# Performance work log

Hardware: AMD Instinct MI355X
Metric: run time of the kernel (lower is better)

The kernel has to match this reference:

```python
import jax, jax.numpy as jnp
import numpy as np

NUM_IN, IN_DIM, NUM_OUT, OUT_DIM, NUM_ROUTING = 1152, 8, 10, 16, 3
BATCH = 256


def squash(v):
    # v: (..., d). scale = |v|^2/(1+|v|^2) * v/|v|
    sq = jnp.sum(v * v, axis=-1, keepdims=True)
    scale = sq / (1.0 + sq)
    return scale * v / jnp.sqrt(sq + 1e-8)


def setup_inputs() -> dict:
    key = jax.random.key(0)
    k1, k2 = jax.random.split(key)
    input_capsules = jax.random.normal(k1, (BATCH, NUM_IN, IN_DIM), dtype=jnp.float32)
    W = jax.random.normal(k2, (NUM_IN, IN_DIM, NUM_OUT, OUT_DIM), dtype=jnp.float32) * 0.01
    return {"input_capsules": input_capsules, "W": W}


def reference(input_capsules, W):
    # u_hat: (b, i, j, o) -- predictions from each input capsule i for output capsule j
    u_hat = jnp.einsum('bid,idjo->bijo', input_capsules, W)
    b = jnp.zeros(u_hat.shape[:3] + (1,), dtype=u_hat.dtype)  # (b, i, j, 1)
    v = None
    for it in range(NUM_ROUTING):
        c = jax.nn.softmax(b, axis=2)                 # coupling coeffs over output capsules j
        s = jnp.sum(c * u_hat, axis=1)                # (b, j, o)
        v = squash(s)                                 # (b, j, o)
        if it < NUM_ROUTING - 1:
            agreement = jnp.sum(u_hat * v[:, None, :, :], axis=-1, keepdims=True)
            b = b + agreement
    return v
```

## Files before the change

### kernel.cpp

```cpp
#include <hip/hip_runtime.h>


#define NUM_IN 1152
#define NUM_OUT 10
#define OUT_DIM 16
#define BATCH 256
#define SLOTS 160
#define ICH_BLK 16
#define NCHUNK (NUM_IN / ICH_BLK)
#define BPB 16
#define NBT (BATCH / BPB)
#define WROW 1280

typedef unsigned int __attribute__((address_space(1))) as1_uint;
typedef unsigned int __attribute__((address_space(3))) as3_uint;
typedef int v2i __attribute__((ext_vector_type(2)));

__device__ __forceinline__ void gll16(const float* g, float* l) {
  __builtin_amdgcn_global_load_lds((const as1_uint*)g, (as3_uint*)l, 16, 0, 0);
}

__device__ __forceinline__ float xor8_sum(float x) {
  int v = __builtin_amdgcn_update_dpp(0, __float_as_int(x), 0x128, 0xF, 0xF, true);
  return x + __int_as_float(v);
}

__device__ __forceinline__ float xor32_sum(float x) {
  v2i r = __builtin_amdgcn_permlane32_swap(__float_as_int(x),
                                           __float_as_int(x), false, false);
  return __int_as_float(r.x) + __int_as_float(r.y);
}

__device__ __forceinline__ float rowsum8_hi(float x) {
  int v;
  v = __builtin_amdgcn_update_dpp(0, __float_as_int(x), 0x114, 0xF, 0xF, true);
  x += __int_as_float(v);
  v = __builtin_amdgcn_update_dpp(0, __float_as_int(x), 0x112, 0xF, 0xF, true);
  x += __int_as_float(v);
  v = __builtin_amdgcn_update_dpp(0, __float_as_int(x), 0x111, 0xF, 0xF, true);
  x += __int_as_float(v);
  return x;
}

__device__ __forceinline__ float rowsum16(float x) {
  int v;
  v = __builtin_amdgcn_update_dpp(0, __float_as_int(x), 0x128, 0xF, 0xF, true);
  x += __int_as_float(v);
  v = __builtin_amdgcn_update_dpp(0, __float_as_int(x), 0x124, 0xF, 0xF, true);
  x += __int_as_float(v);
  v = __builtin_amdgcn_update_dpp(0, __float_as_int(x), 0x122, 0xF, 0xF, true);
  x += __int_as_float(v);
  v = __builtin_amdgcn_update_dpp(0, __float_as_int(x), 0x121, 0xF, 0xF, true);
  x += __int_as_float(v);
  return x;
}

template <int PASS, int R, bool PART>
__device__ __forceinline__ void compute_round(
    const float4 xv[2][2], const float* __restrict__ v0p,
    const float* __restrict__ v1p, float* __restrict__ outp, const float* Wb,
    int b0, int lane, int vbase, size_t obase) {
  constexpr size_t BBS = PART ? (size_t)(NCHUNK * SLOTS) : (size_t)SLOTS;
  const float* wsl = Wb + lane * 4;

  float xd[2][8];
#pragma unroll
  for (int bb = 0; bb < 2; ++bb) {
    xd[bb][0] = xv[bb][0].x; xd[bb][1] = xv[bb][0].y;
    xd[bb][2] = xv[bb][0].z; xd[bb][3] = xv[bb][0].w;
    xd[bb][4] = xv[bb][1].x; xd[bb][5] = xv[bb][1].y;
    xd[bb][6] = xv[bb][1].z; xd[bb][7] = xv[bb][1].w;
  }

  float u[2][5][4];
  float cw[2][5];

#pragma unroll
  for (int jl = 0; jl < 5; ++jl) {
    float ax0 = 0.f, ay0 = 0.f, az0 = 0.f, aw0 = 0.f;
    float ax1 = 0.f, ay1 = 0.f, az1 = 0.f, aw1 = 0.f;
#pragma unroll
    for (int d = 0; d < 8; ++d) {
      const float4 w =
          *reinterpret_cast<const float4*>(wsl + (d * 5 + jl) * 256);
      ax0 = fmaf(xd[0][d], w.x, ax0); ay0 = fmaf(xd[0][d], w.y, ay0);
      az0 = fmaf(xd[0][d], w.z, az0); aw0 = fmaf(xd[0][d], w.w, aw0);
      ax1 = fmaf(xd[1][d], w.x, ax1); ay1 = fmaf(xd[1][d], w.y, ay1);
      az1 = fmaf(xd[1][d], w.z, az1); aw1 = fmaf(xd[1][d], w.w, aw1);
    }
    u[0][jl][0] = ax0; u[0][jl][1] = ay0; u[0][jl][2] = az0; u[0][jl][3] = aw0;
    u[1][jl][0] = ax1; u[1][jl][1] = ay1; u[1][jl][2] = az1; u[1][jl][3] = aw1;
    if (PASS >= 1) {
#pragma unroll
      for (int bb = 0; bb < 2; ++bb) {
        const float4 p = *reinterpret_cast<const float4*>(
            v0p + (b0 + bb) * SLOTS + vbase + jl * 16);
        float lgv = u[bb][jl][0] * p.x + u[bb][jl][1] * p.y +
                    u[bb][jl][2] * p.z + u[bb][jl][3] * p.w;
        if (PASS == 2) {
          const float4 q = *reinterpret_cast<const float4*>(
              v1p + (b0 + bb) * SLOTS + vbase + jl * 16);
          lgv += u[bb][jl][0] * q.x + u[bb][jl][1] * q.y +
                 u[bb][jl][2] * q.z + u[bb][jl][3] * q.w;
        }
        cw[bb][jl] = xor32_sum(xor8_sum(lgv));
      }
    }
  }

  if (PASS == 0) {
#pragma unroll
    for (int bb = 0; bb < 2; ++bb)
#pragma unroll
      for (int jl = 0; jl < 5; ++jl) cw[bb][jl] = 0.1f;
  } else {
#pragma unroll
    for (int bb = 0; bb < 2; ++bb) {
      float m = cw[bb][0];
#pragma unroll
      for (int jl = 1; jl < 5; ++jl) m = fmaxf(m, cw[bb][jl]);
      m = fmaxf(m, __shfl_xor(m, 16));
      float z = 0.f;
#pragma unroll
      for (int jl = 0; jl < 5; ++jl) {
        cw[bb][jl] = __expf(cw[bb][jl] - m);
        z += cw[bb][jl];
      }
      z += __shfl_xor(z, 16);
      const float rz = 1.0f / z;
#pragma unroll
      for (int jl = 0; jl < 5; ++jl) cw[bb][jl] *= rz;
    }
  }

  const bool wr = ((lane & 7) == 7);
#pragma unroll
  for (int jl = 0; jl < 5; ++jl) {
#pragma unroll
    for (int bb = 0; bb < 2; ++bb) {
      const float sx = rowsum8_hi(cw[bb][jl] * u[bb][jl][0]);
      const float sy = rowsum8_hi(cw[bb][jl] * u[bb][jl][1]);
      const float sz = rowsum8_hi(cw[bb][jl] * u[bb][jl][2]);
      const float sw = rowsum8_hi(cw[bb][jl] * u[bb][jl][3]);
      if (wr) {
        if (PART) {
          float4* q =
              reinterpret_cast<float4*>(outp + obase + bb * BBS + jl * 16);
          float4 f = {sx, sy, sz, sw};
          if (R == 1) {
            const float4 o = *q;
            f.x += o.x; f.y += o.y; f.z += o.z; f.w += o.w;
          }
          *q = f;
        } else {
          float* p = outp + obase + bb * BBS + jl * 16;
          atomicAdd(p + 0, sx); atomicAdd(p + 1, sy);
          atomicAdd(p + 2, sz); atomicAdd(p + 3, sw);
        }
      }
    }
  }
}

template <int PASS, bool PART>
__global__ __launch_bounds__(512, 2) void caps_pass(
    const float* __restrict__ x, const float* __restrict__ W,
    const float* __restrict__ v0, const float* __restrict__ v1,
    float* __restrict__ outp) {
  __shared__ float Ws[2][10240];

  const int t = threadIdx.x;
  const int ic = blockIdx.x % NCHUNK;
  const int bt = blockIdx.x / NCHUNK;
  const int i0 = ic * ICH_BLK;

  const int lane = t & 63;
  const int wave = t >> 6;
  const int i_sub = lane & 7;
  const int oq = ((lane >> 3) & 1) | ((lane >> 4) & 2);
  const int jg = (lane >> 4) & 1;
  const int b0 = bt * BPB + wave * 2;
  const int vbase = jg * 80 + oq * 4;

  const float* wg = W + (size_t)i0 * WROW;
#pragma unroll
  for (int k = 0; k < 5; ++k) {
    const int p = t + k * 512;
    const int lp = p & 63;
    const int dj = p >> 6;
    const int d = dj / 5, jl = dj % 5;
    const int g = (lp & 7) * 320 + d * 40 + jl * 4 + ((lp >> 4) & 1) * 20 +
                  ((lp >> 3) & 1) + ((lp >> 5) & 1) * 2;
    gll16(wg + g * 4, &Ws[0][p * 4]);
  }

  float4 xv[2][2][2];
#pragma unroll
  for (int r = 0; r < 2; ++r)
#pragma unroll
    for (int bb = 0; bb < 2; ++bb) {
      const float* px =
          x + ((size_t)(b0 + bb) * NUM_IN + i0 + r * 8 + i_sub) * 8;
      xv[r][bb][0] = *reinterpret_cast<const float4*>(px);
      xv[r][bb][1] = *reinterpret_cast<const float4*>(px + 4);
    }

  __builtin_amdgcn_sched_barrier(0);

#pragma unroll
  for (int k = 0; k < 5; ++k) {
    const int p = t + k * 512;
    const int lp = p & 63;
    const int dj = p >> 6;
    const int d = dj / 5, jl = dj % 5;
    const int g = (lp & 7) * 320 + d * 40 + jl * 4 + ((lp >> 4) & 1) * 20 +
                  ((lp >> 3) & 1) + ((lp >> 5) & 1) * 2;
    gll16(wg + 8 * WROW + g * 4, &Ws[1][p * 4]);
  }
  __builtin_amdgcn_sched_barrier(0);

  const size_t obase =
      PART ? ((size_t)b0 * NCHUNK + ic) * SLOTS + vbase
           : (size_t)b0 * SLOTS + vbase;

  asm volatile("s_waitcnt vmcnt(5)" ::: "memory");
  __builtin_amdgcn_s_barrier();
  compute_round<PASS, 0, PART>(xv[0], v0, v1, outp, &Ws[0][0], b0, lane,
                               vbase, obase);
  asm volatile("s_waitcnt vmcnt(0)" ::: "memory");
  __builtin_amdgcn_s_barrier();
  compute_round<PASS, 1, PART>(xv[1], v0, v1, outp, &Ws[1][0], b0, lane,
                               vbase, obase);
}

__global__ __launch_bounds__(192) void caps_reduce_squash(
    const float* __restrict__ part, float* __restrict__ v_out) {
  const int b = blockIdx.x;
  const int t = threadIdx.x;
  if (t < SLOTS) {
    const float* pb = part + (size_t)b * NCHUNK * SLOTS + t;
    float sv = 0.0f;
#pragma unroll 8
    for (int ic = 0; ic < NCHUNK; ++ic) sv += pb[ic * SLOTS];
    const float sq = rowsum16(sv * sv);
    const float scale = sq / (1.0f + sq) * rsqrtf(sq + 1e-8f);
    v_out[(size_t)b * SLOTS + t] = sv * scale;
  }
}

__global__ __launch_bounds__(192) void caps_squash(const float* s_in,
                                                   float* v_out,
                                                   float* s_zero) {
  const int b = blockIdx.x;
  const int t = threadIdx.x;
  if (t < SLOTS) {
    const float sv = s_in[(size_t)b * SLOTS + t];
    const float sq = rowsum16(sv * sv);
    const float scale = sq / (1.0f + sq) * rsqrtf(sq + 1e-8f);
    v_out[(size_t)b * SLOTS + t] = sv * scale;
    if (s_zero) s_zero[(size_t)b * SLOTS + t] = 0.0f;
  }
}

extern "C" void kernel_launch(void* const* d_in, const int* in_sizes, int n_in,
                              void* d_out, int out_size, void* d_ws,
                              size_t ws_size, hipStream_t stream) {
  const float* x = (const float*)d_in[0];
  const float* W = (const float*)d_in[1];
  float* out = (float*)d_out;

  const size_t part_elems = (size_t)NCHUNK * BATCH * SLOTS;
  const size_t need = (part_elems + 2 * BATCH * SLOTS) * sizeof(float);
  const dim3 pg(NCHUNK * NBT);

  if (ws_size >= need) {
    float* part = (float*)d_ws;
    float* v0 = part + part_elems;
    float* v1 = v0 + BATCH * SLOTS;
    caps_pass<0, true><<<pg, 512, 0, stream>>>(x, W, nullptr, nullptr, part);
    caps_reduce_squash<<<BATCH, 192, 0, stream>>>(part, v0);
    caps_pass<1, true><<<pg, 512, 0, stream>>>(x, W, v0, nullptr, part);
    caps_reduce_squash<<<BATCH, 192, 0, stream>>>(part, v1);
    caps_pass<2, true><<<pg, 512, 0, stream>>>(x, W, v0, v1, part);
    caps_reduce_squash<<<BATCH, 192, 0, stream>>>(part, out);
  } else {
    float* s_buf = (float*)d_ws;
    float* v0 = s_buf + BATCH * SLOTS;
    float* v1 = v0 + BATCH * SLOTS;
    hipMemsetAsync(s_buf, 0, (size_t)BATCH * SLOTS * sizeof(float), stream);
    caps_pass<0, false><<<pg, 512, 0, stream>>>(x, W, nullptr, nullptr, s_buf);
    caps_squash<<<BATCH, 192, 0, stream>>>(s_buf, v0, s_buf);
    caps_pass<1, false><<<pg, 512, 0, stream>>>(x, W, v0, nullptr, s_buf);
    caps_squash<<<BATCH, 192, 0, stream>>>(s_buf, v1, s_buf);
    caps_pass<2, false><<<pg, 512, 0, stream>>>(x, W, v0, v1, s_buf);
    caps_squash<<<BATCH, 192, 0, stream>>>(s_buf, out, nullptr);
  }
}
```

Before: 229.5 us.

## Single-buffer W in LDS, pack u_hat in fp16, raise occupancy to 4 blocks

```diff
diff --git a/kernel.cpp b/kernel.cpp
--- a/kernel.cpp
+++ b/kernel.cpp
@@ -15,6 +15,7 @@
 typedef unsigned int __attribute__((address_space(1))) as1_uint;
 typedef unsigned int __attribute__((address_space(3))) as3_uint;
 typedef int v2i __attribute__((ext_vector_type(2)));
+typedef __fp16 h2 __attribute__((ext_vector_type(2)));
 
 __device__ __forceinline__ void gll16(const float* g, float* l) {
   __builtin_amdgcn_global_load_lds((const as1_uint*)g, (as3_uint*)l, 16, 0, 0);
@@ -57,63 +58,65 @@
 
 template <int PASS, int R, bool PART>
 __device__ __forceinline__ void compute_round(
-    const float4 xv[2][2], const float* __restrict__ v0p,
+    const float* __restrict__ x, const float* __restrict__ v0p,
     const float* __restrict__ v1p, float* __restrict__ outp, const float* Wb,
-    int b0, int lane, int vbase, size_t obase) {
+    int i, int b0, int lane, int vbase, size_t obase) {
   constexpr size_t BBS = PART ? (size_t)(NCHUNK * SLOTS) : (size_t)SLOTS;
   const float* wsl = Wb + lane * 4;
 
-  float xd[2][8];
+  h2 xh[2][4];
 #pragma unroll
   for (int bb = 0; bb < 2; ++bb) {
-    xd[bb][0] = xv[bb][0].x; xd[bb][1] = xv[bb][0].y;
-    xd[bb][2] = xv[bb][0].z; xd[bb][3] = xv[bb][0].w;
-    xd[bb][4] = xv[bb][1].x; xd[bb][5] = xv[bb][1].y;
-    xd[bb][6] = xv[bb][1].z; xd[bb][7] = xv[bb][1].w;
-  }
-
-  float u[2][5][4];
+    const float* px = x + ((size_t)(b0 + bb) * NUM_IN + i) * 8;
+    const float4 a = *reinterpret_cast<const float4*>(px);
+    const float4 c = *reinterpret_cast<const float4*>(px + 4);
+    xh[bb][0] = __builtin_amdgcn_cvt_pkrtz(a.x, a.y);
+    xh[bb][1] = __builtin_amdgcn_cvt_pkrtz(a.z, a.w);
+    xh[bb][2] = __builtin_amdgcn_cvt_pkrtz(c.x, c.y);
+    xh[bb][3] = __builtin_amdgcn_cvt_pkrtz(c.z, c.w);
+  }
+
   float cw[2][5];
-
-#pragma unroll
-  for (int jl = 0; jl < 5; ++jl) {
-    float ax0 = 0.f, ay0 = 0.f, az0 = 0.f, aw0 = 0.f;
-    float ax1 = 0.f, ay1 = 0.f, az1 = 0.f, aw1 = 0.f;
-#pragma unroll
-    for (int d = 0; d < 8; ++d) {
-      const float4 w =
-          *reinterpret_cast<const float4*>(wsl + (d * 5 + jl) * 256);
-      ax0 = fmaf(xd[0][d], w.x, ax0); ay0 = fmaf(xd[0][d], w.y, ay0);
-      az0 = fmaf(xd[0][d], w.z, az0); aw0 = fmaf(xd[0][d], w.w, aw0);
-      ax1 = fmaf(xd[1][d], w.x, ax1); ay1 = fmaf(xd[1][d], w.y, ay1);
-      az1 = fmaf(xd[1][d], w.z, az1); aw1 = fmaf(xd[1][d], w.w, aw1);
+  h2 up[2][5][2];
+
+  if (PASS >= 1) {
+#pragma unroll
+    for (int jl = 0; jl < 5; ++jl) {
+      float ax0 = 0.f, ay0 = 0.f, az0 = 0.f, aw0 = 0.f;
+      float ax1 = 0.f, ay1 = 0.f, az1 = 0.f, aw1 = 0.f;
+#pragma unroll
+      for (int d = 0; d < 8; ++d) {
+        const float4 w =
+            *reinterpret_cast<const float4*>(wsl + (d * 5 + jl) * 256);
+        const float x0 = (float)xh[0][d >> 1][d & 1];
+        const float x1 = (float)xh[1][d >> 1][d & 1];
+        ax0 = fmaf(x0, w.x, ax0); ay0 = fmaf(x0, w.y, ay0);
+        az0 = fmaf(x0, w.z, az0); aw0 = fmaf(x0, w.w, aw0);
+        ax1 = fmaf(x1, w.x, ax1); ay1 = fmaf(x1, w.y, ay1);
+        az1 = fmaf(x1, w.z, az1); aw1 = fmaf(x1, w.w, aw1);
+      }
+      up[0][jl][0] = __builtin_amdgcn_cvt_pkrtz(ax0, ay0);
+      up[0][jl][1] = __builtin_amdgcn_cvt_pkrtz(az0, aw0);
+      up[1][jl][0] = __builtin_amdgcn_cvt_pkrtz(ax1, ay1);
+      up[1][jl][1] = __builtin_amdgcn_cvt_pkrtz(az1, aw1);
+
+      const float4 p0 = *reinterpret_cast<const float4*>(
+          v0p + (b0 + 0) * SLOTS + vbase + jl * 16);
+      const float4 p1 = *reinterpret_cast<const float4*>(
+          v0p + (b0 + 1) * SLOTS + vbase + jl * 16);
+      float l0 = ax0 * p0.x + ay0 * p0.y + az0 * p0.z + aw0 * p0.w;
+      float l1 = ax1 * p1.x + ay1 * p1.y + az1 * p1.z + aw1 * p1.w;
+      if (PASS == 2) {
+        const float4 q0 = *reinterpret_cast<const float4*>(
+            v1p + (b0 + 0) * SLOTS + vbase + jl * 16);
+        const float4 q1 = *reinterpret_cast<const float4*>(
+            v1p + (b0 + 1) * SLOTS + vbase + jl * 16);
+        l0 += ax0 * q0.x + ay0 * q0.y + az0 * q0.z + aw0 * q0.w;
+        l1 += ax1 * q1.x + ay1 * q1.y + az1 * q1.z + aw1 * q1.w;
+      }
+      cw[0][jl] = xor32_sum(xor8_sum(l0));
+      cw[1][jl] = xor32_sum(xor8_sum(l1));
     }
-    u[0][jl][0] = ax0; u[0][jl][1] = ay0; u[0][jl][2] = az0; u[0][jl][3] = aw0;
-    u[1][jl][0] = ax1; u[1][jl][1] = ay1; u[1][jl][2] = az1; u[1][jl][3] = aw1;
-    if (PASS >= 1) {
-#pragma unroll
-      for (int bb = 0; bb < 2; ++bb) {
-        const float4 p = *reinterpret_cast<const float4*>(
-            v0p + (b0 + bb) * SLOTS + vbase + jl * 16);
-        float lgv = u[bb][jl][0] * p.x + u[bb][jl][1] * p.y +
-                    u[bb][jl][2] * p.z + u[bb][jl][3] * p.w;
-        if (PASS == 2) {
-          const float4 q = *reinterpret_cast<const float4*>(
-              v1p + (b0 + bb) * SLOTS + vbase + jl * 16);
-          lgv += u[bb][jl][0] * q.x + u[bb][jl][1] * q.y +
-                 u[bb][jl][2] * q.z + u[bb][jl][3] * q.w;
-        }
-        cw[bb][jl] = xor32_sum(xor8_sum(lgv));
-      }
-    }
-  }
-
-  if (PASS == 0) {
-#pragma unroll
-    for (int bb = 0; bb < 2; ++bb)
-#pragma unroll
-      for (int jl = 0; jl < 5; ++jl) cw[bb][jl] = 0.1f;
-  } else {
 #pragma unroll
     for (int bb = 0; bb < 2; ++bb) {
       float m = cw[bb][0];
@@ -136,38 +139,74 @@
   const bool wr = ((lane & 7) == 7);
 #pragma unroll
   for (int jl = 0; jl < 5; ++jl) {
-#pragma unroll
-    for (int bb = 0; bb < 2; ++bb) {
-      const float sx = rowsum8_hi(cw[bb][jl] * u[bb][jl][0]);
-      const float sy = rowsum8_hi(cw[bb][jl] * u[bb][jl][1]);
-      const float sz = rowsum8_hi(cw[bb][jl] * u[bb][jl][2]);
-      const float sw = rowsum8_hi(cw[bb][jl] * u[bb][jl][3]);
-      if (wr) {
-        if (PART) {
-          float4* q =
-              reinterpret_cast<float4*>(outp + obase + bb * BBS + jl * 16);
-          float4 f = {sx, sy, sz, sw};
-          if (R == 1) {
-            const float4 o = *q;
-            f.x += o.x; f.y += o.y; f.z += o.z; f.w += o.w;
-          }
-          *q = f;
-        } else {
-          float* p = outp + obase + bb * BBS + jl * 16;
-          atomicAdd(p + 0, sx); atomicAdd(p + 1, sy);
-          atomicAdd(p + 2, sz); atomicAdd(p + 3, sw);
+    float u0[4], u1[4];
+    if (PASS == 0) {
+      float ax0 = 0.f, ay0 = 0.f, az0 = 0.f, aw0 = 0.f;
+      float ax1 = 0.f, ay1 = 0.f, az1 = 0.f, aw1 = 0.f;
+#pragma unroll
+      for (int d = 0; d < 8; ++d) {
+        const float4 w =
+            *reinterpret_cast<const float4*>(wsl + (d * 5 + jl) * 256);
+        const float x0 = (float)xh[0][d >> 1][d & 1];
+        const float x1 = (float)xh[1][d >> 1][d & 1];
+        ax0 = fmaf(x0, w.x, ax0); ay0 = fmaf(x0, w.y, ay0);
+        az0 = fmaf(x0, w.z, az0); aw0 = fmaf(x0, w.w, aw0);
+        ax1 = fmaf(x1, w.x, ax1); ay1 = fmaf(x1, w.y, ay1);
+        az1 = fmaf(x1, w.z, az1); aw1 = fmaf(x1, w.w, aw1);
+      }
+      u0[0] = ax0 * 0.1f; u0[1] = ay0 * 0.1f;
+      u0[2] = az0 * 0.1f; u0[3] = aw0 * 0.1f;
+      u1[0] = ax1 * 0.1f; u1[1] = ay1 * 0.1f;
+      u1[2] = az1 * 0.1f; u1[3] = aw1 * 0.1f;
+    } else {
+      u0[0] = cw[0][jl] * (float)up[0][jl][0].x;
+      u0[1] = cw[0][jl] * (float)up[0][jl][0].y;
+      u0[2] = cw[0][jl] * (float)up[0][jl][1].x;
+      u0[3] = cw[0][jl] * (float)up[0][jl][1].y;
+      u1[0] = cw[1][jl] * (float)up[1][jl][0].x;
+      u1[1] = cw[1][jl] * (float)up[1][jl][0].y;
+      u1[2] = cw[1][jl] * (float)up[1][jl][1].x;
+      u1[3] = cw[1][jl] * (float)up[1][jl][1].y;
+    }
+    const float sx0 = rowsum8_hi(u0[0]);
+    const float sy0 = rowsum8_hi(u0[1]);
+    const float sz0 = rowsum8_hi(u0[2]);
+    const float sw0 = rowsum8_hi(u0[3]);
+    const float sx1 = rowsum8_hi(u1[0]);
+    const float sy1 = rowsum8_hi(u1[1]);
+    const float sz1 = rowsum8_hi(u1[2]);
+    const float sw1 = rowsum8_hi(u1[3]);
+    if (wr) {
+      if (PART) {
+        float4* q0 = reinterpret_cast<float4*>(outp + obase + 0 * BBS + jl * 16);
+        float4* q1 = reinterpret_cast<float4*>(outp + obase + 1 * BBS + jl * 16);
+        float4 f0 = {sx0, sy0, sz0, sw0};
+        float4 f1 = {sx1, sy1, sz1, sw1};
+        if (R == 1) {
+          const float4 o0 = *q0, o1 = *q1;
+          f0.x += o0.x; f0.y += o0.y; f0.z += o0.z; f0.w += o0.w;
+          f1.x += o1.x; f1.y += o1.y; f1.z += o1.z; f1.w += o1.w;
         }
+        *q0 = f0;
+        *q1 = f1;
+      } else {
+        float* p0 = outp + obase + 0 * BBS + jl * 16;
+        float* p1 = outp + obase + 1 * BBS + jl * 16;
+        atomicAdd(p0 + 0, sx0); atomicAdd(p0 + 1, sy0);
+        atomicAdd(p0 + 2, sz0); atomicAdd(p0 + 3, sw0);
+        atomicAdd(p1 + 0, sx1); atomicAdd(p1 + 1, sy1);
+        atomicAdd(p1 + 2, sz1); atomicAdd(p1 + 3, sw1);
       }
     }
   }
 }
 
 template <int PASS, bool PART>
-__global__ __launch_bounds__(512, 2) void caps_pass(
+__global__ __launch_bounds__(512, 4) void caps_pass(
     const float* __restrict__ x, const float* __restrict__ W,
     const float* __restrict__ v0, const float* __restrict__ v1,
     float* __restrict__ outp) {
-  __shared__ float Ws[2][10240];
+  __shared__ float Ws[10240];
 
   const int t = threadIdx.x;
   const int ic = blockIdx.x % NCHUNK;
@@ -181,55 +220,44 @@
   const int jg = (lane >> 4) & 1;
   const int b0 = bt * BPB + wave * 2;
   const int vbase = jg * 80 + oq * 4;
+  const size_t obase = PART ? ((size_t)b0 * NCHUNK + ic) * SLOTS + vbase
+                            : (size_t)b0 * SLOTS + vbase;
 
   const float* wg = W + (size_t)i0 * WROW;
+
 #pragma unroll
   for (int k = 0; k < 5; ++k) {
     const int p = t + k * 512;
     const int lp = p & 63;
     const int dj = p >> 6;
-    const int d = dj / 5, jl = dj % 5;
+    const int d = dj / 5, jl = dj - d * 5;
     const int g = (lp & 7) * 320 + d * 40 + jl * 4 + ((lp >> 4) & 1) * 20 +
                   ((lp >> 3) & 1) + ((lp >> 5) & 1) * 2;
-    gll16(wg + g * 4, &Ws[0][p * 4]);
-  }
-
-  float4 xv[2][2][2];
-#pragma unroll
-  for (int r = 0; r < 2; ++r)
-#pragma unroll
-    for (int bb = 0; bb < 2; ++bb) {
-      const float* px =
-          x + ((size_t)(b0 + bb) * NUM_IN + i0 + r * 8 + i_sub) * 8;
-      xv[r][bb][0] = *reinterpret_cast<const float4*>(px);
-      xv[r][bb][1] = *reinterpret_cast<const float4*>(px + 4);
-    }
-
-  __builtin_amdgcn_sched_barrier(0);
+    gll16(wg + g * 4, &Ws[p * 4]);
+  }
+  asm volatile("s_waitcnt vmcnt(0)" ::: "memory");
+  __builtin_amdgcn_s_barrier();
+
+  compute_round<PASS, 0, PART>(x, v0, v1, outp, Ws, i0 + i_sub, b0, lane,
+                               vbase, obase);
+
+  asm volatile("s_waitcnt lgkmcnt(0)" ::: "memory");
+  __builtin_amdgcn_s_barrier();
 
 #pragma unroll
   for (int k = 0; k < 5; ++k) {
     const int p = t + k * 512;
     const int lp = p & 63;
     const int dj = p >> 6;
-    const int d = dj / 5, jl = dj % 5;
+    const int d = dj / 5, jl = dj - d * 5;
     const int g = (lp & 7) * 320 + d * 40 + jl * 4 + ((lp >> 4) & 1) * 20 +
                   ((lp >> 3) & 1) + ((lp >> 5) & 1) * 2;
-    gll16(wg + 8 * WROW + g * 4, &Ws[1][p * 4]);
-  }
-  __builtin_amdgcn_sched_barrier(0);
-
-  const size_t obase =
-      PART ? ((size_t)b0 * NCHUNK + ic) * SLOTS + vbase
-           : (size_t)b0 * SLOTS + vbase;
-
-  asm volatile("s_waitcnt vmcnt(5)" ::: "memory");
-  __builtin_amdgcn_s_barrier();
-  compute_round<PASS, 0, PART>(xv[0], v0, v1, outp, &Ws[0][0], b0, lane,
-                               vbase, obase);
+    gll16(wg + 8 * WROW + g * 4, &Ws[p * 4]);
+  }
   asm volatile("s_waitcnt vmcnt(0)" ::: "memory");
   __builtin_amdgcn_s_barrier();
-  compute_round<PASS, 1, PART>(xv[1], v0, v1, outp, &Ws[1][0], b0, lane,
+
+  compute_round<PASS, 1, PART>(x, v0, v1, outp, Ws, i0 + 8 + i_sub, b0, lane,
                                vbase, obase);
 }
 
```

New measurement: 197.2 us. -14.1%, faster.
